# Kernel optimization log

Hardware: AMD Instinct MI355X
Metric: run time of the kernel (lower is better)

## Reference

```python
import jax, jax.numpy as jnp
import numpy as np

D_MODEL = 1024

def setup_inputs() -> dict:
    key = jax.random.key(0)
    ks = jax.random.split(key, 5)
    s = 1.0 / np.sqrt(D_MODEL)  # torch Linear default init scale-ish
    x = jax.random.normal(ks[0], (4, 2048, D_MODEL), dtype=jnp.float32)
    Wq = jax.random.normal(ks[1], (D_MODEL, D_MODEL), dtype=jnp.float32) * s
    Wk = jax.random.normal(ks[2], (D_MODEL, D_MODEL), dtype=jnp.float32) * s
    Wv = jax.random.normal(ks[3], (D_MODEL, D_MODEL), dtype=jnp.float32) * s
    Wo = jax.random.normal(ks[4], (D_MODEL, D_MODEL), dtype=jnp.float32) * s
    z = jnp.zeros((D_MODEL,), dtype=jnp.float32)
    return {"x": x, "Wq": Wq, "bq": z, "Wk": Wk, "bk": z, "Wv": Wv, "bv": z, "Wo": Wo, "bo": z}

def reference(x, Wq, bq, Wk, bk, Wv, bv, Wo, bo):
    # x: (B, S, D). Single-head causal attention, dropout in eval mode (identity).
    B, S, D = x.shape
    Q = jnp.einsum('bsd,ed->bse', x, Wq) + bq
    K = jnp.einsum('bsd,ed->bse', x, Wk) + bk
    V = jnp.einsum('bsd,ed->bse', x, Wv) + bv
    scores = jnp.einsum('bqd,bkd->bqk', Q, K) / jnp.sqrt(jnp.float32(D))
    causal = jnp.tril(jnp.ones((S, S), dtype=bool))  # (S, S)
    scores = jnp.where(causal, scores, -jnp.inf)
    weights = jax.nn.softmax(scores, axis=-1)
    attended = jnp.einsum('bqk,bkd->bqd', weights, V)
    out = jnp.einsum('bsd,ed->bse', attended, Wo) + bo
    return out
```

## Files before the change

### kernel.cpp

```cpp
#include <hip/hip_runtime.h>
#include <cstdint>
#include <cstddef>


#define D_MODEL 1024
#define SEQ     2048
#define BATCH   4

typedef unsigned short u16;
typedef __bf16 bf16_t;
typedef bf16_t bf16x8 __attribute__((ext_vector_type(8)));
typedef float  f32x4  __attribute__((ext_vector_type(4)));
typedef u16    u16x4  __attribute__((ext_vector_type(4)));

__device__ __forceinline__ u16 f2bf(float x) {
  union { float f; uint32_t u; } v; v.f = x;
  uint32_t r = v.u + 0x7fffu + ((v.u >> 16) & 1u);
  return (u16)(r >> 16);
}
__device__ __forceinline__ float bf2f(u16 u) {
  union { uint32_t u; float f; } v; v.u = ((uint32_t)u) << 16;
  return v.f;
}

__device__ __forceinline__ void gload_lds16(const u16* g, u16* l) {
  __builtin_amdgcn_global_load_lds((__attribute__((address_space(1))) void*)g,
                                   (__attribute__((address_space(3))) void*)l,
                                   16, 0, 0);
}

__device__ __forceinline__ void gemm_core(const u16* __restrict__ Ablk,
                                          const u16* __restrict__ Bblk,
                                          int lda, int ldb, int ksteps,
                                          u16* As, u16* Bs,
                                          f32x4 acc[4][4]) {
  const int tid  = threadIdx.x;
  const int wave = tid >> 6, lane = tid & 63;
  const int wr = (wave >> 1) * 64, wc = (wave & 1) * 64;
  const int frow = lane & 15, fk = (lane >> 4) * 8;
  const int ch0 = wave * 64 + lane;
  const int ch1 = 256 + ch0;
  const int m0 = ch0 >> 2, k80 = (ch0 & 3) * 8;
  const int m1 = ch1 >> 2, k81 = (ch1 & 3) * 8;

  for (int kt = 0; kt < ksteps; ++kt) {
    __syncthreads();
    const int kb = kt * 32;
    gload_lds16(Ablk + m0 * lda + kb + k80, As + ch0 * 8);
    gload_lds16(Ablk + m1 * lda + kb + k81, As + ch1 * 8);
    gload_lds16(Bblk + m0 * ldb + kb + k80, Bs + ch0 * 8);
    gload_lds16(Bblk + m1 * ldb + kb + k81, Bs + ch1 * 8);
    asm volatile("s_waitcnt vmcnt(0)" ::: "memory");
    __syncthreads();

    bf16x8 af[4], bf[4];
#pragma unroll
    for (int i = 0; i < 4; ++i)
      af[i] = *(const bf16x8*)(As + (wr + i * 16 + frow) * 32 + fk);
#pragma unroll
    for (int j = 0; j < 4; ++j)
      bf[j] = *(const bf16x8*)(Bs + (wc + j * 16 + frow) * 32 + fk);
#pragma unroll
    for (int i = 0; i < 4; ++i)
#pragma unroll
      for (int j = 0; j < 4; ++j)
        acc[i][j] = __builtin_amdgcn_mfma_f32_16x16x32_bf16(af[i], bf[j], acc[i][j], 0, 0, 0);
  }
}

__global__ __launch_bounds__(256) void cvt_x_kernel(const float4* __restrict__ src,
                                                    u16* __restrict__ dst) {
  const int i = blockIdx.x * 256 + threadIdx.x;
  float4 v = src[i];
  u16x4 o = {f2bf(v.x), f2bf(v.y), f2bf(v.z), f2bf(v.w)};
  *(u16x4*)(dst + (size_t)i * 4) = o;
}

__global__ __launch_bounds__(256) void cvt_w_kernel(const float4* __restrict__ wq,
                                                    const float4* __restrict__ wk,
                                                    const float4* __restrict__ wv,
                                                    const float4* __restrict__ wo,
                                                    u16* __restrict__ dst) {
  const int z = blockIdx.y;
  const float4* s = (z == 0) ? wq : (z == 1) ? wk : (z == 2) ? wv : wo;
  const int i = blockIdx.x * 256 + threadIdx.x;
  float4 v = s[i];
  u16x4 o = {f2bf(v.x), f2bf(v.y), f2bf(v.z), f2bf(v.w)};
  *(u16x4*)(dst + (size_t)z * D_MODEL * D_MODEL + (size_t)i * 4) = o;
}

__global__ __launch_bounds__(256) void proj_kernel(const u16* __restrict__ xb,
                                                   const u16* __restrict__ Wq,
                                                   const u16* __restrict__ Wk,
                                                   const u16* __restrict__ Wv,
                                                   const float* __restrict__ bq,
                                                   const float* __restrict__ bk,
                                                   const float* __restrict__ bv,
                                                   u16* __restrict__ Qb,
                                                   u16* __restrict__ Kb,
                                                   u16* __restrict__ Vb) {
  __shared__ __align__(16) u16 As[128 * 32];
  __shared__ __align__(16) u16 Bs[128 * 32];
  const int z = blockIdx.z;
  const u16*   W    = (z == 0) ? Wq : (z == 1) ? Wk : Wv;
  const float* bias = (z == 0) ? bq : (z == 1) ? bk : bv;
  u16*         out  = (z == 0) ? Qb : (z == 1) ? Kb : Vb;
  const int row0 = blockIdx.x * 128, col0 = blockIdx.y * 128;
  f32x4 acc[4][4] = {};
  gemm_core(xb + (size_t)row0 * D_MODEL, W + (size_t)col0 * D_MODEL,
            D_MODEL, D_MODEL, 32, As, Bs, acc);
  const int lane = threadIdx.x & 63, wave = threadIdx.x >> 6;
  const int wr = (wave >> 1) * 64, wc = (wave & 1) * 64;
  const int cl = lane & 15, rl = (lane >> 4) * 4;
#pragma unroll
  for (int j = 0; j < 4; ++j) {
    const int col = col0 + wc + j * 16 + cl;
    const float bb = bias[col];
#pragma unroll
    for (int i = 0; i < 4; ++i)
#pragma unroll
      for (int r = 0; r < 4; ++r) {
        const int row = row0 + wr + i * 16 + rl + r;
        out[(size_t)row * D_MODEL + col] = f2bf(acc[i][j][r] + bb);
      }
  }
}

__global__ void transpose_kernel(const u16* __restrict__ Vb, u16* __restrict__ Vt) {
  __shared__ u16 tile[32][33];
  const int b = blockIdx.z;
  const int s0 = blockIdx.x * 32, d0 = blockIdx.y * 32;
  const int tx = threadIdx.x, ty = threadIdx.y;
#pragma unroll
  for (int r = 0; r < 4; ++r)
    tile[ty + r * 8][tx] = Vb[(size_t)(b * SEQ + s0 + ty + r * 8) * D_MODEL + d0 + tx];
  __syncthreads();
#pragma unroll
  for (int r = 0; r < 4; ++r)
    Vt[(size_t)b * D_MODEL * SEQ + (size_t)(d0 + ty + r * 8) * SEQ + s0 + tx] = tile[tx][ty + r * 8];
}

__global__ __launch_bounds__(256) void scores_kernel(const u16* __restrict__ Qb,
                                                     const u16* __restrict__ Kb,
                                                     u16* __restrict__ Sb) {
  const int qi = blockIdx.x, ji = blockIdx.y, b = blockIdx.z;
  if (ji > qi) return;
  __shared__ __align__(16) u16 As[128 * 32];
  __shared__ __align__(16) u16 Bs[128 * 32];
  const u16* A  = Qb + (size_t)(b * SEQ + qi * 128) * D_MODEL;
  const u16* Bt = Kb + (size_t)(b * SEQ + ji * 128) * D_MODEL;
  f32x4 acc[4][4] = {};
  gemm_core(A, Bt, D_MODEL, D_MODEL, 32, As, Bs, acc);
  u16* out = Sb + (size_t)b * SEQ * SEQ;
  const int lane = threadIdx.x & 63, wave = threadIdx.x >> 6;
  const int wr = (wave >> 1) * 64, wc = (wave & 1) * 64;
  const int cl = lane & 15, rl = (lane >> 4) * 4;
#pragma unroll
  for (int i = 0; i < 4; ++i)
#pragma unroll
    for (int r = 0; r < 4; ++r) {
      const int q = qi * 128 + wr + i * 16 + rl + r;
#pragma unroll
      for (int j = 0; j < 4; ++j) {
        const int jj = ji * 128 + wc + j * 16 + cl;
        out[(size_t)q * SEQ + jj] = (jj <= q) ? f2bf(acc[i][j][r] * 0.03125f)
                                              : (u16)0xFF80;
      }
    }
}

__global__ __launch_bounds__(256) void softmax_kernel(u16* __restrict__ Sb) {
  const int wave = threadIdx.x >> 6, lane = threadIdx.x & 63;
  const int row = blockIdx.x * 4 + wave;
  const int b = row >> 11, q = row & 2047;
  u16* p = Sb + (size_t)b * SEQ * SEQ + (size_t)q * SEQ;
  const int jend = ((q >> 7) + 1) << 7;
  float vals[32];
  float m = -3.4e38f;
#pragma unroll
  for (int t = 0; t < 32; ++t) {
    float v = -__builtin_inff();
    if (t * 64 < jend) v = bf2f(p[t * 64 + lane]);
    vals[t] = v;
    m = fmaxf(m, v);
  }
#pragma unroll
  for (int off = 32; off; off >>= 1) m = fmaxf(m, __shfl_xor(m, off));
  float l = 0.f;
#pragma unroll
  for (int t = 0; t < 32; ++t) { float e = __expf(vals[t] - m); vals[t] = e; l += e; }
#pragma unroll
  for (int off = 32; off; off >>= 1) l += __shfl_xor(l, off);
  const float inv = 1.f / l;
#pragma unroll
  for (int t = 0; t < 32; ++t)
    if (t * 64 < jend) p[t * 64 + lane] = f2bf(vals[t] * inv);
}

__global__ __launch_bounds__(256) void pv_kernel(const u16* __restrict__ Pb,
                                                 const u16* __restrict__ Vt,
                                                 u16* __restrict__ Ab) {
  __shared__ __align__(16) u16 As[128 * 32];
  __shared__ __align__(16) u16 Bs[128 * 32];
  const int qt = blockIdx.x, dt = blockIdx.y, b = blockIdx.z;
  const u16* A  = Pb + (size_t)b * SEQ * SEQ + (size_t)(qt * 128) * SEQ;
  const u16* Bt = Vt + (size_t)b * D_MODEL * SEQ + (size_t)(dt * 128) * SEQ;
  f32x4 acc[4][4] = {};
  gemm_core(A, Bt, SEQ, SEQ, (qt + 1) * 4, As, Bs, acc);
  const int lane = threadIdx.x & 63, wave = threadIdx.x >> 6;
  const int wr = (wave >> 1) * 64, wc = (wave & 1) * 64;
  const int cl = lane & 15, rl = (lane >> 4) * 4;
#pragma unroll
  for (int i = 0; i < 4; ++i)
#pragma unroll
    for (int r = 0; r < 4; ++r) {
      const int row = b * SEQ + qt * 128 + wr + i * 16 + rl + r;
#pragma unroll
      for (int j = 0; j < 4; ++j) {
        const int col = dt * 128 + wc + j * 16 + cl;
        Ab[(size_t)row * D_MODEL + col] = f2bf(acc[i][j][r]);
      }
    }
}

__global__ __launch_bounds__(256) void out_kernel(const u16* __restrict__ Ab,
                                                  const u16* __restrict__ Wo,
                                                  const float* __restrict__ bo,
                                                  float* __restrict__ Out) {
  __shared__ __align__(16) u16 As[128 * 32];
  __shared__ __align__(16) u16 Bs[128 * 32];
  const int row0 = blockIdx.x * 128, col0 = blockIdx.y * 128;
  f32x4 acc[4][4] = {};
  gemm_core(Ab + (size_t)row0 * D_MODEL, Wo + (size_t)col0 * D_MODEL,
            D_MODEL, D_MODEL, 32, As, Bs, acc);
  const int lane = threadIdx.x & 63, wave = threadIdx.x >> 6;
  const int wr = (wave >> 1) * 64, wc = (wave & 1) * 64;
  const int cl = lane & 15, rl = (lane >> 4) * 4;
#pragma unroll
  for (int j = 0; j < 4; ++j) {
    const int col = col0 + wc + j * 16 + cl;
    const float bb = bo[col];
#pragma unroll
    for (int i = 0; i < 4; ++i)
#pragma unroll
      for (int r = 0; r < 4; ++r) {
        const int row = row0 + wr + i * 16 + rl + r;
        Out[(size_t)row * D_MODEL + col] = acc[i][j][r] + bb;
      }
  }
}

extern "C" void kernel_launch(void* const* d_in, const int* in_sizes, int n_in,
                              void* d_out, int out_size, void* d_ws, size_t ws_size,
                              hipStream_t stream) {
  const float* x  = (const float*)d_in[0];
  const float* Wq = (const float*)d_in[1];
  const float* bq = (const float*)d_in[2];
  const float* Wk = (const float*)d_in[3];
  const float* bk = (const float*)d_in[4];
  const float* Wv = (const float*)d_in[5];
  const float* bv = (const float*)d_in[6];
  const float* Wo = (const float*)d_in[7];
  const float* bo = (const float*)d_in[8];
  float* out = (float*)d_out;
  char* ws = (char*)d_ws;

  u16* xb = (u16*)(ws);
  u16* Wb = (u16*)(ws + (16u << 20));
  u16* Qb = (u16*)(ws + (24u << 20));
  u16* Kb = (u16*)(ws + (40u << 20));
  u16* Vb = (u16*)(ws + (56u << 20));
  u16* Vt = (u16*)(ws + (72u << 20));
  u16* Sb = (u16*)(ws + (88u << 20));
  u16* Ab = (u16*)(ws + (56u << 20));

  cvt_x_kernel<<<8192, 256, 0, stream>>>((const float4*)x, xb);
  cvt_w_kernel<<<dim3(1024, 4), 256, 0, stream>>>((const float4*)Wq, (const float4*)Wk,
                                                  (const float4*)Wv, (const float4*)Wo, Wb);
  proj_kernel<<<dim3(64, 8, 3), 256, 0, stream>>>(xb, Wb, Wb + (1u << 20), Wb + (2u << 20),
                                                  bq, bk, bv, Qb, Kb, Vb);
  transpose_kernel<<<dim3(64, 32, 4), dim3(32, 8), 0, stream>>>(Vb, Vt);
  scores_kernel<<<dim3(16, 16, 4), 256, 0, stream>>>(Qb, Kb, Sb);
  softmax_kernel<<<2048, 256, 0, stream>>>(Sb);
  pv_kernel<<<dim3(16, 8, 4), 256, 0, stream>>>(Sb, Vt, Ab);
  out_kernel<<<dim3(64, 8), 256, 0, stream>>>(Ab, Wb + (3u << 20), bo, out);
}
```

Measured before the change: 317.5 us.

## Swizzle LDS layout, merge conversion kernels, compact causal grid, vectorize softmax

```diff
diff --git a/kernel.cpp b/kernel.cpp
--- a/kernel.cpp
+++ b/kernel.cpp
@@ -37,11 +37,19 @@
   const int tid  = threadIdx.x;
   const int wave = tid >> 6, lane = tid & 63;
   const int wr = (wave >> 1) * 64, wc = (wave & 1) * 64;
-  const int frow = lane & 15, fk = (lane >> 4) * 8;
+  const int frow = lane & 15, kc = lane >> 4;
   const int ch0 = wave * 64 + lane;
   const int ch1 = 256 + ch0;
-  const int m0 = ch0 >> 2, k80 = (ch0 & 3) * 8;
-  const int m1 = ch1 >> 2, k81 = (ch1 & 3) * 8;
+  const int m0 = ch0 >> 2, k80 = (((ch0 & 3) ^ ((m0 >> 1) & 3))) * 8;
+  const int m1 = ch1 >> 2, k81 = (((ch1 & 3) ^ ((m1 >> 1) & 3))) * 8;
+  int aoff[4], boff[4];
+#pragma unroll
+  for (int i = 0; i < 4; ++i) {
+    const int ra = wr + i * 16 + frow;
+    aoff[i] = (ra * 4 + (kc ^ ((ra >> 1) & 3))) * 8;
+    const int rb = wc + i * 16 + frow;
+    boff[i] = (rb * 4 + (kc ^ ((rb >> 1) & 3))) * 8;
+  }
 
   for (int kt = 0; kt < ksteps; ++kt) {
     __syncthreads();
@@ -55,11 +63,9 @@
 
     bf16x8 af[4], bf[4];
 #pragma unroll
-    for (int i = 0; i < 4; ++i)
-      af[i] = *(const bf16x8*)(As + (wr + i * 16 + frow) * 32 + fk);
-#pragma unroll
-    for (int j = 0; j < 4; ++j)
-      bf[j] = *(const bf16x8*)(Bs + (wc + j * 16 + frow) * 32 + fk);
+    for (int i = 0; i < 4; ++i) af[i] = *(const bf16x8*)(As + aoff[i]);
+#pragma unroll
+    for (int j = 0; j < 4; ++j) bf[j] = *(const bf16x8*)(Bs + boff[j]);
 #pragma unroll
     for (int i = 0; i < 4; ++i)
 #pragma unroll
@@ -68,25 +74,24 @@
   }
 }
 
-__global__ __launch_bounds__(256) void cvt_x_kernel(const float4* __restrict__ src,
-                                                    u16* __restrict__ dst) {
+__global__ __launch_bounds__(256) void cvt_kernel(const float4* __restrict__ x,
+                                                  const float4* __restrict__ wq,
+                                                  const float4* __restrict__ wk,
+                                                  const float4* __restrict__ wv,
+                                                  const float4* __restrict__ wo,
+                                                  u16* __restrict__ dst) {
   const int i = blockIdx.x * 256 + threadIdx.x;
-  float4 v = src[i];
+  float4 v;
+  if (i < 2097152) {
+    v = x[i];
+  } else {
+    const int j = i - 2097152;
+    const int w = j >> 18;
+    const float4* s = (w == 0) ? wq : (w == 1) ? wk : (w == 2) ? wv : wo;
+    v = s[j & 262143];
+  }
   u16x4 o = {f2bf(v.x), f2bf(v.y), f2bf(v.z), f2bf(v.w)};
   *(u16x4*)(dst + (size_t)i * 4) = o;
-}
-
-__global__ __launch_bounds__(256) void cvt_w_kernel(const float4* __restrict__ wq,
-                                                    const float4* __restrict__ wk,
-                                                    const float4* __restrict__ wv,
-                                                    const float4* __restrict__ wo,
-                                                    u16* __restrict__ dst) {
-  const int z = blockIdx.y;
-  const float4* s = (z == 0) ? wq : (z == 1) ? wk : (z == 2) ? wv : wo;
-  const int i = blockIdx.x * 256 + threadIdx.x;
-  float4 v = s[i];
-  u16x4 o = {f2bf(v.x), f2bf(v.y), f2bf(v.z), f2bf(v.w)};
-  *(u16x4*)(dst + (size_t)z * D_MODEL * D_MODEL + (size_t)i * 4) = o;
 }
 
 __global__ __launch_bounds__(256) void proj_kernel(const u16* __restrict__ xb,
@@ -143,8 +148,11 @@
 __global__ __launch_bounds__(256) void scores_kernel(const u16* __restrict__ Qb,
                                                      const u16* __restrict__ Kb,
                                                      u16* __restrict__ Sb) {
-  const int qi = blockIdx.x, ji = blockIdx.y, b = blockIdx.z;
-  if (ji > qi) return;
+  const int t = blockIdx.x, b = blockIdx.z;
+  int qi = (int)((sqrtf(8.0f * t + 1.0f) - 1.0f) * 0.5f);
+  if ((qi + 1) * (qi + 2) / 2 <= t) ++qi;
+  if (qi * (qi + 1) / 2 > t) --qi;
+  const int ji = t - qi * (qi + 1) / 2;
   __shared__ __align__(16) u16 As[128 * 32];
   __shared__ __align__(16) u16 Bs[128 * 32];
   const u16* A  = Qb + (size_t)(b * SEQ + qi * 128) * D_MODEL;
@@ -178,11 +186,20 @@
   float vals[32];
   float m = -3.4e38f;
 #pragma unroll
-  for (int t = 0; t < 32; ++t) {
-    float v = -__builtin_inff();
-    if (t * 64 < jend) v = bf2f(p[t * 64 + lane]);
-    vals[t] = v;
-    m = fmaxf(m, v);
+  for (int t = 0; t < 8; ++t) {
+    const int idx = t * 256 + lane * 4;
+    if (idx < jend) {
+      u16x4 v = *(const u16x4*)(p + idx);
+#pragma unroll
+      for (int r = 0; r < 4; ++r) {
+        const float f = bf2f(v[r]);
+        vals[t * 4 + r] = f;
+        m = fmaxf(m, f);
+      }
+    } else {
+#pragma unroll
+      for (int r = 0; r < 4; ++r) vals[t * 4 + r] = -__builtin_inff();
+    }
   }
 #pragma unroll
   for (int off = 32; off; off >>= 1) m = fmaxf(m, __shfl_xor(m, off));
@@ -193,8 +210,14 @@
   for (int off = 32; off; off >>= 1) l += __shfl_xor(l, off);
   const float inv = 1.f / l;
 #pragma unroll
-  for (int t = 0; t < 32; ++t)
-    if (t * 64 < jend) p[t * 64 + lane] = f2bf(vals[t] * inv);
+  for (int t = 0; t < 8; ++t) {
+    const int idx = t * 256 + lane * 4;
+    if (idx < jend) {
+      u16x4 o = {f2bf(vals[t * 4 + 0] * inv), f2bf(vals[t * 4 + 1] * inv),
+                 f2bf(vals[t * 4 + 2] * inv), f2bf(vals[t * 4 + 3] * inv)};
+      *(u16x4*)(p + idx) = o;
+    }
+  }
 }
 
 __global__ __launch_bounds__(256) void pv_kernel(const u16* __restrict__ Pb,
@@ -202,7 +225,7 @@
                                                  u16* __restrict__ Ab) {
   __shared__ __align__(16) u16 As[128 * 32];
   __shared__ __align__(16) u16 Bs[128 * 32];
-  const int qt = blockIdx.x, dt = blockIdx.y, b = blockIdx.z;
+  const int qt = 15 - blockIdx.x, dt = blockIdx.y, b = blockIdx.z;
   const u16* A  = Pb + (size_t)b * SEQ * SEQ + (size_t)(qt * 128) * SEQ;
   const u16* Bt = Vt + (size_t)b * D_MODEL * SEQ + (size_t)(dt * 128) * SEQ;
   f32x4 acc[4][4] = {};
@@ -274,13 +297,13 @@
   u16* Sb = (u16*)(ws + (88u << 20));
   u16* Ab = (u16*)(ws + (56u << 20));
 
-  cvt_x_kernel<<<8192, 256, 0, stream>>>((const float4*)x, xb);
-  cvt_w_kernel<<<dim3(1024, 4), 256, 0, stream>>>((const float4*)Wq, (const float4*)Wk,
-                                                  (const float4*)Wv, (const float4*)Wo, Wb);
+  cvt_kernel<<<12288, 256, 0, stream>>>((const float4*)x, (const float4*)Wq,
+                                        (const float4*)Wk, (const float4*)Wv,
+                                        (const float4*)Wo, xb);
   proj_kernel<<<dim3(64, 8, 3), 256, 0, stream>>>(xb, Wb, Wb + (1u << 20), Wb + (2u << 20),
                                                   bq, bk, bv, Qb, Kb, Vb);
   transpose_kernel<<<dim3(64, 32, 4), dim3(32, 8), 0, stream>>>(Vb, Vt);
-  scores_kernel<<<dim3(16, 16, 4), 256, 0, stream>>>(Qb, Kb, Sb);
+  scores_kernel<<<dim3(136, 1, 4), 256, 0, stream>>>(Qb, Kb, Sb);
   softmax_kernel<<<2048, 256, 0, stream>>>(Sb);
   pv_kernel<<<dim3(16, 8, 4), 256, 0, stream>>>(Sb, Vt, Ab);
   out_kernel<<<dim3(64, 8), 256, 0, stream>>>(Ab, Wb + (3u << 20), bo, out);
```

After: 293.4 us. 1.08x faster.
